# Performance work log

Hardware: AMD Instinct MI355X
Metric: run time of the kernel (lower is better)

The kernel has to match this reference:

```python
import jax, jax.numpy as jnp
import numpy as np

B, CIN, HW = 4096, 60, 8
CW = 32            # conv_width
EMB = 512          # embedding_size / GRU hidden
COR = 1            # cor_dim
T = 50             # out_size


def setup_inputs() -> dict:
    key = jax.random.key(0)
    ks = jax.random.split(key, 12)
    s = lambda *sh: 1.0 / np.sqrt(sh[-1])
    inp = {
        "x": jax.random.normal(ks[0], (B, CIN, HW, HW), jnp.float32),
        "conv_w": jax.random.normal(ks[1], (CW, CIN, 3, 3), jnp.float32) * 0.02,
        "conv_b": jnp.zeros((CW,), jnp.float32),
        "fc_w": jax.random.normal(ks[2], (EMB, CW * 6 * 6), jnp.float32) * (1.0 / np.sqrt(CW * 36)),
        "fc_b": jnp.zeros((EMB,), jnp.float32),
        "w_ih": jax.random.normal(ks[3], (3 * EMB, COR), jnp.float32) * (1.0 / np.sqrt(EMB)),
        "b_ih": jnp.zeros((3 * EMB,), jnp.float32),
        "w_hh": jax.random.normal(ks[4], (3 * EMB, EMB), jnp.float32) * (1.0 / np.sqrt(EMB)),
        "b_hh": jnp.zeros((3 * EMB,), jnp.float32),
        "dec_w": jax.random.normal(ks[5], (COR, EMB), jnp.float32) * (1.0 / np.sqrt(EMB)),
        "dec_b": jnp.zeros((COR,), jnp.float32),
    }
    return inp


def _forward(x, conv_w, conv_b, fc_w, fc_b, w_ih, b_ih, w_hh, b_hh, dec_w, dec_b):
    # encoder: 3x3 VALID conv on 8x8 -> (B, CW, 6, 6), relu, flatten, fc, relu
    h = jax.lax.conv_general_dilated(
        x, conv_w, window_strides=(1, 1), padding="VALID",
        dimension_numbers=("NCHW", "OIHW", "NCHW"))
    h = jax.nn.relu(h + conv_b[None, :, None, None])
    emb = h.reshape(x.shape[0], -1) @ fc_w.T + fc_b        # (B, EMB)
    emb = jax.nn.relu(emb)

    # decoder: sequential 1-step GRU, feeding its own output back
    dec0 = jnp.zeros((x.shape[0], COR), x.dtype)

    def step(carry, _):
        hprev, inp = carry
        gi = inp @ w_ih.T + b_ih                            # (B, 3*EMB)
        gh = hprev @ w_hh.T + b_hh                          # (B, 3*EMB)
        gi_r, gi_z, gi_n = jnp.split(gi, 3, axis=-1)
        gh_r, gh_z, gh_n = jnp.split(gh, 3, axis=-1)
        r = jax.nn.sigmoid(gi_r + gh_r)
        z = jax.nn.sigmoid(gi_z + gh_z)
        n = jnp.tanh(gi_n + r * gh_n)
        hnew = (1.0 - z) * n + z * hprev
        out = hnew @ dec_w.T + dec_b                        # (B, COR)
        return (hnew, out), out

    _, outs = jax.lax.scan(step, (emb, dec0), None, length=T)
    # outs: (T, B, COR) -> (B, T, COR)
    return jnp.transpose(outs, (1, 0, 2))


def reference(x, conv_w, conv_b, fc_w, fc_b, w_ih, b_ih, w_hh, b_hh, dec_w, dec_b):
    return _forward(x, conv_w, conv_b, fc_w, fc_b, w_ih, b_ih, w_hh, b_hh, dec_w, dec_b)
```

## Files before the change

### kernel.cpp

```cpp
#include <hip/hip_runtime.h>
#include <math.h>

#define B_    4096
#define CIN   60
#define CW    32
#define EMB   512
#define TSTEP 50
#define KFC   1152
#define G3    1536

typedef _Float16 f16;
typedef _Float16 f16x4 __attribute__((ext_vector_type(4)));
typedef _Float16 f16x8 __attribute__((ext_vector_type(8)));
typedef float    f32x4 __attribute__((ext_vector_type(4)));
typedef float    f32x16 __attribute__((ext_vector_type(16)));

typedef __attribute__((address_space(3))) void       lds_void_t;
typedef __attribute__((address_space(1))) const void g_void_t;

__device__ __forceinline__ float sigmoid_fast(float x){ return 1.f/(1.f+__expf(-x)); }
__device__ __forceinline__ float tanh_fast(float x){ float e=__expf(2.f*x); return 1.f-2.f/(e+1.f); }

__global__ void prep_kernel(const float* __restrict__ w_hh, f16* __restrict__ w16T,
                            const float* __restrict__ conv_w, f16* __restrict__ w16c,
                            const float* __restrict__ fc_w, f16* __restrict__ fcp16,
                            const float* __restrict__ dec_b, float* __restrict__ out)
{
    int i = blockIdx.x * 256 + threadIdx.x;
    if (i < G3 * EMB) {
        int R = i >> 9, k = i & 511;
        w16T[(size_t)(k >> 3) * 12288 + R * 8 + (k & 7)] = (f16)w_hh[i];
        return;
    }
    i -= G3 * EMB;
    if (i < 9 * 32 * 64) {
        int khkw = i >> 11, r = i & 2047, co = r >> 6, ci = r & 63;
        float v = (ci < CIN) ? conv_w[(co * CIN + ci) * 9 + khkw] : 0.f;
        int dst = khkw * 2048 + co * 64 + (((ci >> 3) ^ (co & 7)) << 3) + (ci & 7);
        w16c[dst] = (f16)v;
        return;
    }
    i -= 9 * 32 * 64;
    if (i < EMB * KFC) {
        int e = i / KFC, j = i % KFC;
        int co = j & 31, pos = j >> 5;
        fcp16[i] = (f16)fc_w[e * KFC + co * 36 + pos];
        return;
    }
    i -= EMB * KFC;
    if (i < B_ * TSTEP) out[i] = dec_b[0];
}

__global__ __launch_bounds__(256) void conv_mfma(
    const float* __restrict__ x, const f16* __restrict__ w16c,
    const float* __restrict__ conv_b, f16* __restrict__ outc)
{
    __shared__ __align__(16) f16 xt[8 * 64 * 64];
    int tid = threadIdx.x, wid = tid >> 6, lane = tid & 63;
    int b0 = blockIdx.x * 8;
    int mhalf = wid >> 1, nt = wid & 1;
    int lrow = lane & 15, kgrp = lane >> 4;
    int co = nt * 16 + lrow;

    f16x8 bfr[18];
    #pragma unroll
    for (int ks = 0; ks < 18; ks++) {
        int khkw = ks >> 1, c = (ks & 1) * 4 + kgrp;
        bfr[ks] = *(const f16x8*)((const char*)w16c +
                    khkw * 4096 + co * 128 + ((c ^ (co & 7)) << 4));
    }
    float cb = conv_b[co];

    #pragma unroll
    for (int bt = 0; bt < 3; bt++) {
        float ra[10][4];
        #pragma unroll
        for (int j = 0; j < 10; j++) {
            int idx = (bt * 10 + j) * 4 + wid;
            int img = idx / 15, cq = idx - img * 15;
            const float* xp = x + ((size_t)(b0 + img) * CIN + cq * 4) * 64 + lane;
            ra[j][0] = xp[0]; ra[j][1] = xp[64]; ra[j][2] = xp[128]; ra[j][3] = xp[192];
        }
        #pragma unroll
        for (int j = 0; j < 10; j++) {
            int idx = (bt * 10 + j) * 4 + wid;
            int img = idx / 15, cq = idx - img * 15;
            f16x4 v = { (f16)ra[j][0], (f16)ra[j][1], (f16)ra[j][2], (f16)ra[j][3] };
            int off = img * 8192 + lane * 128 + (((cq >> 1) ^ (lane & 7)) << 4) + (cq & 1) * 8;
            *(f16x4*)((char*)xt + off) = v;
        }
    }
    #pragma unroll
    for (int i = 0; i < 2; i++) {
        int s = i * 256 + tid, img = s >> 6, px = s & 63;
        int off = img * 8192 + px * 128 + ((7 ^ (px & 7)) << 4) + 8;
        *(f16x4*)((char*)xt + off) = f16x4{0, 0, 0, 0};
    }
    __syncthreads();

    int imgs[9], pxb[9];
    #pragma unroll
    for (int i = 0; i < 9; i++) {
        int row = mhalf * 144 + i * 16 + lrow;
        int img = (row * 1821) >> 16, pos = row - img * 36;
        int oh = (pos * 43) >> 8, ow = pos - oh * 6;
        imgs[i] = img; pxb[i] = oh * 8 + ow;
    }

    f32x4 acc[9];
    #pragma unroll
    for (int i = 0; i < 9; i++) acc[i] = f32x4{0, 0, 0, 0};

    #pragma unroll
    for (int ks = 0; ks < 18; ks++) {
        int khkw = ks >> 1;
        int kh = khkw / 3, kw = khkw - kh * 3;
        int c = (ks & 1) * 4 + kgrp;
        #pragma unroll
        for (int i = 0; i < 9; i++) {
            int px = pxb[i] + kh * 8 + kw;
            f16x8 af = *(const f16x8*)((const char*)xt +
                         imgs[i] * 8192 + px * 128 + ((c ^ (px & 7)) << 4));
            acc[i] = __builtin_amdgcn_mfma_f32_16x16x32_f16(af, bfr[ks], acc[i], 0, 0, 0);
        }
    }

    #pragma unroll
    for (int i = 0; i < 9; i++) {
        #pragma unroll
        for (int j = 0; j < 4; j++) {
            int row = mhalf * 144 + i * 16 + kgrp * 4 + j;
            int img = (row * 1821) >> 16, pos = row - img * 36;
            float v = fmaxf(acc[i][j] + cb, 0.f);
            outc[(size_t)(b0 + img) * KFC + pos * 32 + co] = (f16)v;
        }
    }
}

__global__ __launch_bounds__(256) void fc_mfma(
    const f16* __restrict__ A, const f16* __restrict__ Bm,
    const float* __restrict__ bias, f16* __restrict__ h16T)
{
    __shared__ __align__(16) f16 As[2][64 * 64];
    __shared__ __align__(16) f16 Bs[2][64 * 64];
    int tid = threadIdx.x, wid = tid >> 6, lane = tid & 63;
    int wr = wid >> 1, wc = wid & 1;
    int col = lane & 31, half = lane >> 5;
    int m0 = blockIdx.y * 64, n0 = blockIdx.x * 64;

    const f16* gA[2]; const f16* gB[2];
    #pragma unroll
    for (int i = 0; i < 2; i++) {
        int q = i * 256 + tid, row = q >> 3, cp = q & 7, c = cp ^ (row & 7);
        gA[i] = A  + (size_t)(m0 + row) * KFC + c * 8;
        gB[i] = Bm + (size_t)(n0 + row) * KFC + c * 8;
    }
    auto stage = [&](int buf, int k0) {
        #pragma unroll
        for (int i = 0; i < 2; i++)
            __builtin_amdgcn_global_load_lds((const g_void_t*)(gA[i] + k0),
                (lds_void_t*)((char*)&As[buf][0] + (i * 256 + wid * 64) * 16), 16, 0, 0);
        #pragma unroll
        for (int i = 0; i < 2; i++)
            __builtin_amdgcn_global_load_lds((const g_void_t*)(gB[i] + k0),
                (lds_void_t*)((char*)&Bs[buf][0] + (i * 256 + wid * 64) * 16), 16, 0, 0);
    };

    f32x16 acc;
    #pragma unroll
    for (int r = 0; r < 16; r++) acc[r] = 0.f;

    stage(0, 0); stage(1, 64);
    int cur = 0, arow = wr * 32 + col, brow = wc * 32 + col;
    #pragma unroll 1
    for (int kt = 0; kt < 17; kt++) {
        asm volatile("s_waitcnt vmcnt(4)" ::: "memory");
        __builtin_amdgcn_s_barrier();
        __builtin_amdgcn_sched_barrier(0);
        __builtin_amdgcn_s_setprio(1);
        #pragma unroll
        for (int kk = 0; kk < 4; kk++) {
            int ch = kk * 2 + half;
            f16x8 af = *(const f16x8*)&As[cur][arow * 64 + ((ch ^ (arow & 7)) << 3)];
            f16x8 bf = *(const f16x8*)&Bs[cur][brow * 64 + ((ch ^ (brow & 7)) << 3)];
            acc = __builtin_amdgcn_mfma_f32_32x32x16_f16(af, bf, acc, 0, 0, 0);
        }
        __builtin_amdgcn_s_setprio(0);
        __builtin_amdgcn_sched_barrier(0);
        __builtin_amdgcn_s_barrier();
        if (kt < 16) stage(cur, (kt + 2) * 64);
        cur ^= 1;
    }
    asm volatile("s_waitcnt vmcnt(0)" ::: "memory");
    __builtin_amdgcn_s_barrier();
    __builtin_amdgcn_sched_barrier(0);
    #pragma unroll
    for (int kk = 0; kk < 4; kk++) {
        int ch = kk * 2 + half;
        f16x8 af = *(const f16x8*)&As[cur][arow * 64 + ((ch ^ (arow & 7)) << 3)];
        f16x8 bf = *(const f16x8*)&Bs[cur][brow * 64 + ((ch ^ (brow & 7)) << 3)];
        acc = __builtin_amdgcn_mfma_f32_32x32x16_f16(af, bf, acc, 0, 0, 0);
    }

    #pragma unroll
    for (int r = 0; r < 16; r++) {
        int m = m0 + wr * 32 + (r & 3) + 8 * (r >> 2) + 4 * half;
        int n = n0 + wc * 32 + col;
        float v = fmaxf(acc[r] + bias[n], 0.f);
        h16T[(size_t)(n >> 3) * 32768 + m * 8 + (n & 7)] = (f16)v;
    }
}

__global__ __launch_bounds__(256, 2) void gru_step(
    const f16* __restrict__ hin, f16* __restrict__ hout,
    const f16* __restrict__ w16T, const float* __restrict__ b_hh,
    const float* __restrict__ w_ih, const float* __restrict__ b_ih,
    const float* __restrict__ dec_w, float* __restrict__ out, int t)
{
    __shared__ __align__(16) f16 Alds[2][8 * 64 * 8];
    __shared__ __align__(16) f16 Blds[2][8 * 192 * 8];
    int tid = threadIdx.x, wid = tid >> 6, lane = tid & 63;
    int wr = wid >> 1, wc = wid & 1;
    int col = lane & 31, half = lane >> 5;

    int xc = blockIdx.x & 7, rb = blockIdx.x >> 3;
    int mg = xc * 8 + (rb & 7), eg = rb >> 3;
    int m0 = mg * 64, e0 = eg * 64;
    int e  = e0 + wc * 32 + col;

    float wir = w_ih[e], wiz = w_ih[EMB + e], win = w_ih[2 * EMB + e];
    float bir = b_ih[e], biz = b_ih[EMB + e], bin_ = b_ih[2 * EMB + e];
    float bhr = b_hh[e], bhz = b_hh[EMB + e], bhn = b_hh[2 * EMB + e];
    float dw  = dec_w[e];
    int tprev = (t > 0) ? t - 1 : 0;
    float prevv[16], hpv[16];
    #pragma unroll
    for (int r = 0; r < 16; r++) {
        int m = m0 + wr * 32 + (r & 3) + 8 * (r >> 2) + 4 * half;
        float pv = out[(size_t)m * TSTEP + tprev];
        prevv[r] = (t > 0) ? pv : 0.f;
        hpv[r]   = (float)hin[(size_t)(e >> 3) * 32768 + m * 8 + (e & 7)];
    }

    const f16* gA[2]; const f16* gB[6];
    #pragma unroll
    for (int i = 0; i < 2; i++) {
        int cell = i * 256 + tid, kc = cell >> 6, m = cell & 63;
        gA[i] = hin + (size_t)kc * 32768 + (m0 + m) * 8;
    }
    #pragma unroll
    for (int i = 0; i < 6; i++) {
        int cell = i * 256 + tid, kc = cell / 192, row = cell - kc * 192;
        int g = row >> 6, c = row & 63;
        gB[i] = w16T + (size_t)kc * 12288 + (g * 512 + e0 + c) * 8;
    }
    auto stage = [&](int buf, int kt) {
        #pragma unroll
        for (int i = 0; i < 2; i++)
            __builtin_amdgcn_global_load_lds(
                (const g_void_t*)(gA[i] + (size_t)kt * 8 * 32768),
                (lds_void_t*)((char*)&Alds[buf][0] + (i * 256 + wid * 64) * 16), 16, 0, 0);
        #pragma unroll
        for (int i = 0; i < 6; i++)
            __builtin_amdgcn_global_load_lds(
                (const g_void_t*)(gB[i] + (size_t)kt * 8 * 12288),
                (lds_void_t*)((char*)&Blds[buf][0] + (i * 256 + wid * 64) * 16), 16, 0, 0);
    };

    f32x16 acc[3];
    #pragma unroll
    for (int g = 0; g < 3; g++)
        #pragma unroll
        for (int r = 0; r < 16; r++) acc[g][r] = 0.f;

    stage(0, 0); stage(1, 1);
    int cur = 0;
    #pragma unroll 1
    for (int kt = 0; kt < 8; kt++) {
        if (kt < 7) asm volatile("s_waitcnt vmcnt(8)" ::: "memory");
        else        asm volatile("s_waitcnt vmcnt(0)" ::: "memory");
        __builtin_amdgcn_s_barrier();
        __builtin_amdgcn_sched_barrier(0);
        __builtin_amdgcn_s_setprio(1);
        #pragma unroll
        for (int kk = 0; kk < 4; kk++) {
            int kc = kk * 2 + half;
            f16x8 af = *(const f16x8*)&Alds[cur][(kc * 64 + wr * 32 + col) * 8];
            #pragma unroll
            for (int g = 0; g < 3; g++) {
                f16x8 bf = *(const f16x8*)&Blds[cur][(kc * 192 + g * 64 + wc * 32 + col) * 8];
                acc[g] = __builtin_amdgcn_mfma_f32_32x32x16_f16(af, bf, acc[g], 0, 0, 0);
            }
        }
        __builtin_amdgcn_s_setprio(0);
        __builtin_amdgcn_sched_barrier(0);
        __builtin_amdgcn_s_barrier();
        if (kt < 6) stage(cur, kt + 2);
        cur ^= 1;
    }

    #pragma unroll
    for (int r = 0; r < 16; r++) {
        int m = m0 + wr * 32 + (r & 3) + 8 * (r >> 2) + 4 * half;
        float prev = prevv[r];
        float gr = acc[0][r] + bhr + fmaf(prev, wir, bir);
        float gz = acc[1][r] + bhz + fmaf(prev, wiz, biz);
        float gn = fmaf(prev, win, bin_);
        float rr = sigmoid_fast(gr), zz = sigmoid_fast(gz);
        float nn = tanh_fast(fmaf(rr, acc[2][r] + bhn, gn));
        float hn = fmaf(zz, hpv[r] - nn, nn);
        hout[(size_t)(e >> 3) * 32768 + m * 8 + (e & 7)] = (f16)hn;
        float v = hn * dw;
        v += __shfl_xor(v, 1);  v += __shfl_xor(v, 2);
        v += __shfl_xor(v, 4);  v += __shfl_xor(v, 8);
        v += __shfl_xor(v, 16);
        if (col == 0) atomicAdd(&out[(size_t)m * TSTEP + t], v);
    }
}

extern "C" void kernel_launch(void* const* d_in, const int* in_sizes, int n_in,
                              void* d_out, int out_size, void* d_ws, size_t ws_size,
                              hipStream_t stream)
{
    const float* x      = (const float*)d_in[0];
    const float* conv_w = (const float*)d_in[1];
    const float* conv_b = (const float*)d_in[2];
    const float* fc_w   = (const float*)d_in[3];
    const float* fc_b   = (const float*)d_in[4];
    const float* w_ih   = (const float*)d_in[5];
    const float* b_ih   = (const float*)d_in[6];
    const float* w_hh   = (const float*)d_in[7];
    const float* b_hh   = (const float*)d_in[8];
    const float* dec_w  = (const float*)d_in[9];
    const float* dec_b  = (const float*)d_in[10];
    float* out = (float*)d_out;

    char* ws = (char*)d_ws;
    f16*  convbuf16 = (f16*)ws;
    f16*  h16_a     = (f16*)(ws + 9437184);
    f16*  h16_b     = (f16*)(ws + 13631488);
    f16*  w16T      = (f16*)(ws + 17825792);
    f16*  w16c      = (f16*)(ws + 19398656);
    f16*  fcp16     = (f16*)(ws + 19435520);

    int prep_n = G3 * EMB + 9 * 32 * 64 + EMB * KFC + B_ * TSTEP;
    prep_kernel<<<(prep_n + 255) / 256, 256, 0, stream>>>(
        w_hh, w16T, conv_w, w16c, fc_w, fcp16, dec_b, out);

    conv_mfma<<<B_ / 8, 256, 0, stream>>>(x, w16c, conv_b, convbuf16);
    fc_mfma<<<dim3(EMB / 64, B_ / 64), 256, 0, stream>>>(convbuf16, fcp16, fc_b, h16_a);

    for (int t = 0; t < TSTEP; t++) {
        const f16* hi = (t & 1) ? h16_b : h16_a;
        f16*       ho = (t & 1) ? h16_a : h16_b;
        gru_step<<<512, 256, 0, stream>>>(
            hi, ho, w16T, b_hh, w_ih, b_ih, dec_w, out, t);
    }
}
```

Before: 808.6 us.

## Deepen GRU step K-loop pipeline to a 4-stage ring with smaller K tiles

After: 833.7 us. +3.1%, slower.

```diff
diff --git a/kernel.cpp b/kernel.cpp
--- a/kernel.cpp
+++ b/kernel.cpp
@@ -217,8 +217,8 @@
     const float* __restrict__ w_ih, const float* __restrict__ b_ih,
     const float* __restrict__ dec_w, float* __restrict__ out, int t)
 {
-    __shared__ __align__(16) f16 Alds[2][8 * 64 * 8];
-    __shared__ __align__(16) f16 Blds[2][8 * 192 * 8];
+    __shared__ __align__(16) f16 Alds[4][4 * 64 * 8];
+    __shared__ __align__(16) f16 Blds[4][4 * 192 * 8];
     int tid = threadIdx.x, wid = tid >> 6, lane = tid & 63;
     int wr = wid >> 1, wc = wid & 1;
     int col = lane & 31, half = lane >> 5;
@@ -241,29 +241,26 @@
         prevv[r] = (t > 0) ? pv : 0.f;
         hpv[r]   = (float)hin[(size_t)(e >> 3) * 32768 + m * 8 + (e & 7)];
     }
-
-    const f16* gA[2]; const f16* gB[6];
-    #pragma unroll
-    for (int i = 0; i < 2; i++) {
-        int cell = i * 256 + tid, kc = cell >> 6, m = cell & 63;
-        gA[i] = hin + (size_t)kc * 32768 + (m0 + m) * 8;
-    }
-    #pragma unroll
-    for (int i = 0; i < 6; i++) {
-        int cell = i * 256 + tid, kc = cell / 192, row = cell - kc * 192;
+    __builtin_amdgcn_sched_barrier(0);
+
+    int kclA = tid >> 6, mA = tid & 63;
+    const f16* gAbase = hin + ((size_t)kclA << 15) + (m0 + mA) * 8;
+    const f16* gBbase[3];
+    #pragma unroll
+    for (int i = 0; i < 3; i++) {
+        int cell = i * 256 + tid;
+        int kcl = cell / 192, row = cell - kcl * 192;
         int g = row >> 6, c = row & 63;
-        gB[i] = w16T + (size_t)kc * 12288 + (g * 512 + e0 + c) * 8;
+        gBbase[i] = w16T + (size_t)kcl * 12288 + (g * 512 + e0 + c) * 8;
     }
     auto stage = [&](int buf, int kt) {
-        #pragma unroll
-        for (int i = 0; i < 2; i++)
+        __builtin_amdgcn_global_load_lds(
+            (const g_void_t*)(gAbase + (size_t)kt * 4 * 32768),
+            (lds_void_t*)((char*)&Alds[buf][0] + wid * 64 * 16), 16, 0, 0);
+        #pragma unroll
+        for (int i = 0; i < 3; i++)
             __builtin_amdgcn_global_load_lds(
-                (const g_void_t*)(gA[i] + (size_t)kt * 8 * 32768),
-                (lds_void_t*)((char*)&Alds[buf][0] + (i * 256 + wid * 64) * 16), 16, 0, 0);
-        #pragma unroll
-        for (int i = 0; i < 6; i++)
-            __builtin_amdgcn_global_load_lds(
-                (const g_void_t*)(gB[i] + (size_t)kt * 8 * 12288),
+                (const g_void_t*)(gBbase[i] + (size_t)kt * 4 * 12288),
                 (lds_void_t*)((char*)&Blds[buf][0] + (i * 256 + wid * 64) * 16), 16, 0, 0);
     };
 
@@ -273,17 +270,20 @@
         #pragma unroll
         for (int r = 0; r < 16; r++) acc[g][r] = 0.f;
 
-    stage(0, 0); stage(1, 1);
+    stage(0, 0); stage(1, 1); stage(2, 2);
     int cur = 0;
     #pragma unroll 1
-    for (int kt = 0; kt < 8; kt++) {
-        if (kt < 7) asm volatile("s_waitcnt vmcnt(8)" ::: "memory");
-        else        asm volatile("s_waitcnt vmcnt(0)" ::: "memory");
+    for (int kt = 0; kt < 16; kt++) {
         __builtin_amdgcn_s_barrier();
+        if (kt < 13) stage((kt + 3) & 3, kt + 3);
+        if      (kt < 13) asm volatile("s_waitcnt vmcnt(12)" ::: "memory");
+        else if (kt == 13) asm volatile("s_waitcnt vmcnt(8)" ::: "memory");
+        else if (kt == 14) asm volatile("s_waitcnt vmcnt(4)" ::: "memory");
+        else               asm volatile("s_waitcnt vmcnt(0)" ::: "memory");
         __builtin_amdgcn_sched_barrier(0);
         __builtin_amdgcn_s_setprio(1);
         #pragma unroll
-        for (int kk = 0; kk < 4; kk++) {
+        for (int kk = 0; kk < 2; kk++) {
             int kc = kk * 2 + half;
             f16x8 af = *(const f16x8*)&Alds[cur][(kc * 64 + wr * 32 + col) * 8];
             #pragma unroll
@@ -294,9 +294,7 @@
         }
         __builtin_amdgcn_s_setprio(0);
         __builtin_amdgcn_sched_barrier(0);
-        __builtin_amdgcn_s_barrier();
-        if (kt < 6) stage(cur, kt + 2);
-        cur ^= 1;
+        cur = (cur + 1) & 3;
     }
 
     #pragma unroll
```
